# Performance work log

Hardware: AMD Instinct MI355X
Metric: run time of the kernel (lower is better)

The kernel has to match this reference:

```python
import jax, jax.numpy as jnp
import numpy as np
import math

B, T, C = 2, 1024, 1024
NEMBD = 1024
NATTN = 1024
NHEAD = 16
CTX = 1024
HS = NATTN // NHEAD          # head size = 64
ROT = HS // 2                # rotary dims = 32


def rotate_half(x):
    x1, x2 = x[..., : x.shape[-1] // 2], x[..., x.shape[-1] // 2 :]
    return jnp.concatenate((-x2, x1), axis=-1)


def setup_inputs() -> dict:
    key = jax.random.key(0)
    ks = jax.random.split(key, 16)
    s = 0.02
    inp = {
        "x": jax.random.normal(ks[0], (B, T, C), dtype=jnp.float32),
        # time-decay params (torch inits them to ones; add noise for a nontrivial test)
        "time_w": 1.0 + s * jax.random.normal(ks[1], (NHEAD, CTX), dtype=jnp.float32),
        "time_alpha": 1.0 + s * jax.random.normal(ks[2], (NHEAD, 1, CTX), dtype=jnp.float32),
        "time_beta": 1.0 + s * jax.random.normal(ks[3], (NHEAD, CTX, 1), dtype=jnp.float32),
        "time_gamma": 1.0 + s * jax.random.normal(ks[4], (CTX, 1), dtype=jnp.float32),
        # projections (stored as (in, out) for x @ W)
        "Wq": s * jax.random.normal(ks[5], (NEMBD, NATTN), dtype=jnp.float32),
        "bq": s * jax.random.normal(ks[6], (NATTN,), dtype=jnp.float32),
        "Wk": s * jax.random.normal(ks[7], (NEMBD, NATTN), dtype=jnp.float32),
        "bk": s * jax.random.normal(ks[8], (NATTN,), dtype=jnp.float32),
        "Wv": s * jax.random.normal(ks[9], (NEMBD, NATTN), dtype=jnp.float32),
        "bv": s * jax.random.normal(ks[10], (NATTN,), dtype=jnp.float32),
        # 1x1 conv over head channels: (out_head, in_head)
        "Wmix": s * jax.random.normal(ks[11], (NHEAD, NHEAD), dtype=jnp.float32),
        "Wo": s * jax.random.normal(ks[12], (NATTN, NEMBD), dtype=jnp.float32),
        "bo": s * jax.random.normal(ks[13], (NEMBD,), dtype=jnp.float32),
    }
    return inp


def reference(x, time_w, time_alpha, time_beta, time_gamma,
              Wq, bq, Wk, bk, Wv, bv, Wmix, Wo, bo):
    Bx, Tx, Cx = x.shape
    TT = CTX

    # --- relative time-decay weight matrix (H, T, T) ---
    w = jnp.pad(time_w, ((0, 0), (0, TT)))          # (H, 2TT)
    w = jnp.tile(w, (1, TT))                        # (H, 2TT*TT)
    w = w[:, :-TT].reshape(NHEAD, TT, 2 * TT - 1)
    w = w[:, :, TT - 1:]                            # (H, TT, TT)
    w = w[:, :Tx, :Tx] * time_alpha[:, :, :Tx] * time_beta[:, :Tx, :]

    # --- time shift of the first half of channels ---
    half = Cx // 2
    x_shift = jnp.pad(x[:, :, :half], ((0, 0), (1, 0), (0, 0)))[:, :Tx, :]
    xs = jnp.concatenate([x_shift, x[:, :, half:]], axis=-1)

    # --- q/k/v projections -> (B, H, T, hs) ---
    q = (xs @ Wq + bq).reshape(Bx, Tx, NHEAD, HS).transpose(0, 2, 1, 3)
    k = (xs @ Wk + bk).reshape(Bx, Tx, NHEAD, HS).transpose(0, 2, 1, 3)
    v = (xs @ Wv + bv).reshape(Bx, Tx, NHEAD, HS).transpose(0, 2, 1, 3)

    # --- rotary on the first ROT dims of each head (base = ctx_len) ---
    qr, q_pass = q[..., :ROT], q[..., ROT:]
    kr, k_pass = k[..., :ROT], k[..., ROT:]
    inv_freq = 1.0 / (jnp.float32(CTX) ** (jnp.arange(0, ROT, 2, dtype=jnp.float32) / ROT))
    t = jnp.arange(Tx, dtype=jnp.float32)
    freqs = t[:, None] * inv_freq[None, :]          # (T, ROT/2)
    emb = jnp.concatenate((freqs, freqs), axis=-1)  # (T, ROT)
    cos, sin = jnp.cos(emb), jnp.sin(emb)
    qr = qr * cos + rotate_half(qr) * sin
    kr = kr * cos + rotate_half(kr) * sin
    q = jnp.concatenate((qr, q_pass), axis=-1)
    k = jnp.concatenate((kr, k_pass), axis=-1)

    # --- attention with time decay and cross-head 1x1 mix ---
    att = jnp.einsum('bhtd,bhsd->bhts', q, k) * (1.0 / math.sqrt(HS))
    att = jax.nn.softmax(att, axis=-1)
    att = att * w[None]                              # (B,H,T,T) * (1,H,T,T)
    att = jnp.einsum('gh,bhts->bgts', Wmix, att)     # 1x1 conv over head channel
    y = jnp.einsum('bhts,bhsd->bhtd', att, v)
    y = y.transpose(0, 2, 1, 3).reshape(Bx, Tx, NATTN)
    return (y @ Wo + bo) * time_gamma[:Tx, :]
```

## Files before the change

kernel.cpp:

```cpp
#include <hip/hip_runtime.h>

typedef unsigned short u16;
typedef __attribute__((ext_vector_type(8))) short bf16x8;
typedef __attribute__((ext_vector_type(4))) float f32x4;

#define MFMA(a,b,c) __builtin_amdgcn_mfma_f32_16x16x32_bf16(a,b,c,0,0,0)

__device__ __forceinline__ float b2f(u16 u){
  union { unsigned int i; float f; } v; v.i = ((unsigned int)u)<<16; return v.f;
}
__device__ __forceinline__ u16 f2b(float f){
  union { float f; unsigned int i; } v; v.f = f;
  unsigned int r = (v.i + 0x7FFFu + ((v.i>>16)&1u))>>16;
  return (u16)r;
}

__global__ __launch_bounds__(256) void k_pre(
    const float* __restrict__ x,
    const float* __restrict__ Wq, const float* __restrict__ Wk,
    const float* __restrict__ Wv, const float* __restrict__ Wo,
    u16* __restrict__ xs, u16* __restrict__ WT, u16* __restrict__ WoT)
{
  int bid = blockIdx.x;
  int tid = threadIdx.x;
  if (bid < 1024){
    int idx = bid*256 + tid;
    size_t e = (size_t)idx*8;
    int c = (int)(e & 1023);
    int t = (int)((e>>10)&1023);
    float4 f0 = {0.f,0.f,0.f,0.f}, f1 = {0.f,0.f,0.f,0.f};
    const float* src = nullptr;
    if (c < 512){ if (t > 0) src = x + e - 1024; }
    else        { src = x + e; }
    if (src){ f0 = *(const float4*)src; f1 = *(const float4*)(src+4); }
    u16 o[8];
    o[0]=f2b(f0.x); o[1]=f2b(f0.y); o[2]=f2b(f0.z); o[3]=f2b(f0.w);
    o[4]=f2b(f1.x); o[5]=f2b(f1.y); o[6]=f2b(f1.z); o[7]=f2b(f1.w);
    *(uint4*)(xs + e) = *(const uint4*)o;
    return;
  }
  int z  = (bid-1024)>>8;
  int rc = (bid-1024)&255;
  const float* src = (z==0)?Wq:((z==1)?Wk:((z==2)?Wv:Wo));
  u16* dst = (z==3)? WoT : (WT + (size_t)z*1048576);
  int c0 = (rc&15)*64, r0 = (rc>>4)*64;
  __shared__ u16 tile[64][72];
  int r = tid>>2, cc = (tid&3)*16;
  const float* sp = src + (size_t)(r0+r)*1024 + c0+cc;
  float4 a0 = *(const float4*)(sp);
  float4 a1 = *(const float4*)(sp+4);
  float4 a2 = *(const float4*)(sp+8);
  float4 a3 = *(const float4*)(sp+12);
  tile[r][cc+0]=f2b(a0.x); tile[r][cc+1]=f2b(a0.y); tile[r][cc+2]=f2b(a0.z); tile[r][cc+3]=f2b(a0.w);
  tile[r][cc+4]=f2b(a1.x); tile[r][cc+5]=f2b(a1.y); tile[r][cc+6]=f2b(a1.z); tile[r][cc+7]=f2b(a1.w);
  tile[r][cc+8]=f2b(a2.x); tile[r][cc+9]=f2b(a2.y); tile[r][cc+10]=f2b(a2.z); tile[r][cc+11]=f2b(a2.w);
  tile[r][cc+12]=f2b(a3.x); tile[r][cc+13]=f2b(a3.y); tile[r][cc+14]=f2b(a3.z); tile[r][cc+15]=f2b(a3.w);
  __syncthreads();
  int c = tid>>2, rr = (tid&3)*16;
  uint4 o0,o1; u16* p0=(u16*)&o0; u16* p1=(u16*)&o1;
  #pragma unroll
  for (int i=0;i<8;i++){ p0[i]=tile[rr+i][c]; p1[i]=tile[rr+8+i][c]; }
  *(uint4*)(dst + (size_t)(c0+c)*1024 + r0+rr)   = o0;
  *(uint4*)(dst + (size_t)(c0+c)*1024 + r0+rr+8) = o1;
}

__global__ __launch_bounds__(256) void k_gemm_qkv(
    const u16* __restrict__ A, const u16* __restrict__ Bt,
    const float* __restrict__ bq, const float* __restrict__ bk, const float* __restrict__ bv,
    u16* __restrict__ qb, u16* __restrict__ kb, u16* __restrict__ vT)
{
  __shared__ u16 As[128*40];
  __shared__ u16 Bs[128*40];
  const int n0 = blockIdx.x*128, m0 = blockIdx.y*128;
  const int tid = threadIdx.x, lane = tid&63, wave = tid>>6;
  const int quad = lane>>4, l16 = lane&15;
  const int wm = (wave>>1)*64, wn = (wave&1)*64;
  f32x4 zero = {0.f,0.f,0.f,0.f};
  f32x4 acc[4][4];
  #pragma unroll
  for (int i=0;i<4;i++)
    #pragma unroll
    for (int j=0;j<4;j++) acc[i][j] = zero;
  const int row = tid>>1, kk = (tid&1)*16;
  const u16* pa = A  + (size_t)(m0+row)*1024 + kk;
  const u16* pb = Bt + (size_t)(n0+row)*1024 + kk;
  for (int k0=0;k0<1024;k0+=32){
    __syncthreads();
    uint4 a0 = *(const uint4*)(pa); uint4 a1 = *(const uint4*)(pa+8);
    uint4 b0 = *(const uint4*)(pb); uint4 b1 = *(const uint4*)(pb+8);
    pa += 32; pb += 32;
    *(uint4*)&As[row*40+kk] = a0; *(uint4*)&As[row*40+kk+8] = a1;
    *(uint4*)&Bs[row*40+kk] = b0; *(uint4*)&Bs[row*40+kk+8] = b1;
    __syncthreads();
    bf16x8 af[4], bfr[4];
    #pragma unroll
    for (int mt=0;mt<4;mt++) af[mt]  = *(const bf16x8*)&As[(wm+mt*16+l16)*40 + quad*8];
    #pragma unroll
    for (int nt=0;nt<4;nt++) bfr[nt] = *(const bf16x8*)&Bs[(wn+nt*16+l16)*40 + quad*8];
    #pragma unroll
    for (int mt=0;mt<4;mt++)
      #pragma unroll
      for (int nt=0;nt<4;nt++)
        acc[mt][nt] = MFMA(af[mt], bfr[nt], acc[mt][nt]);
  }
  const int colbase = n0 + wn;
  const int which = colbase>>10;
  const int nn0 = colbase & 1023;
  const int h = nn0>>6;
  const float* barr = (which==0)?bq:((which==1)?bk:bv);
  float bias[4];
  #pragma unroll
  for (int nt=0;nt<4;nt++) bias[nt] = barr[nn0 + nt*16 + l16];
  if (which == 2){
    #pragma unroll
    for (int mt=0;mt<4;mt++)
      #pragma unroll
      for (int r=0;r<4;r++){
        int m = m0 + wm + mt*16 + quad*4 + r;
        int bb = m>>10, t = m&1023;
        size_t base = (size_t)(bb*16+h)*65536 + t;
        #pragma unroll
        for (int nt=0;nt<4;nt++){
          int d = nt*16 + l16;
          vT[base + (size_t)d*1024] = f2b(acc[mt][nt][r] + bias[nt]);
        }
      }
  } else {
    const float scale = (which==0)?0.125f:1.0f;
    u16* dst = (which==0)? qb : kb;
    const float e = exp2f(-0.625f*(float)l16);
    #pragma unroll
    for (int mt=0;mt<4;mt++)
      #pragma unroll
      for (int r=0;r<4;r++){
        int m = m0 + wm + mt*16 + quad*4 + r;
        int bb = m>>10, t = m&1023;
        float f = (float)t * e;
        float cs = cosf(f), sn = sinf(f);
        float x0 = acc[mt][0][r] + bias[0];
        float x1 = acc[mt][1][r] + bias[1];
        float v0 = (x0*cs - x1*sn)*scale;
        float v1 = (x1*cs + x0*sn)*scale;
        float v2 = (acc[mt][2][r] + bias[2])*scale;
        float v3 = (acc[mt][3][r] + bias[3])*scale;
        size_t ob = (((size_t)(bb*16+h))*1024 + (size_t)t)*64 + l16;
        dst[ob]    = f2b(v0);
        dst[ob+16] = f2b(v1);
        dst[ob+32] = f2b(v2);
        dst[ob+48] = f2b(v3);
      }
  }
}

__global__ __launch_bounds__(256) void k_gemm_out(
    const u16* __restrict__ A, const u16* __restrict__ Bt,
    const float* __restrict__ bo, const float* __restrict__ gamma, float* __restrict__ out)
{
  __shared__ u16 As[128*40];
  __shared__ u16 Bs[128*40];
  const int n0 = blockIdx.x*128, m0 = blockIdx.y*128;
  const int tid = threadIdx.x, lane = tid&63, wave = tid>>6;
  const int quad = lane>>4, l16 = lane&15;
  const int wm = (wave>>1)*64, wn = (wave&1)*64;
  f32x4 zero = {0.f,0.f,0.f,0.f};
  f32x4 acc[4][4];
  #pragma unroll
  for (int i=0;i<4;i++)
    #pragma unroll
    for (int j=0;j<4;j++) acc[i][j] = zero;
  const int row = tid>>1, kk = (tid&1)*16;
  const u16* pa = A  + (size_t)(m0+row)*1024 + kk;
  const u16* pb = Bt + (size_t)(n0+row)*1024 + kk;
  for (int k0=0;k0<1024;k0+=32){
    __syncthreads();
    uint4 a0 = *(const uint4*)(pa); uint4 a1 = *(const uint4*)(pa+8);
    uint4 b0 = *(const uint4*)(pb); uint4 b1 = *(const uint4*)(pb+8);
    pa += 32; pb += 32;
    *(uint4*)&As[row*40+kk] = a0; *(uint4*)&As[row*40+kk+8] = a1;
    *(uint4*)&Bs[row*40+kk] = b0; *(uint4*)&Bs[row*40+kk+8] = b1;
    __syncthreads();
    bf16x8 af[4], bfr[4];
    #pragma unroll
    for (int mt=0;mt<4;mt++) af[mt]  = *(const bf16x8*)&As[(wm+mt*16+l16)*40 + quad*8];
    #pragma unroll
    for (int nt=0;nt<4;nt++) bfr[nt] = *(const bf16x8*)&Bs[(wn+nt*16+l16)*40 + quad*8];
    #pragma unroll
    for (int mt=0;mt<4;mt++)
      #pragma unroll
      for (int nt=0;nt<4;nt++)
        acc[mt][nt] = MFMA(af[mt], bfr[nt], acc[mt][nt]);
  }
  #pragma unroll
  for (int mt=0;mt<4;mt++)
    #pragma unroll
    for (int nt=0;nt<4;nt++){
      int colg = n0 + wn + nt*16 + l16;
      float bias = bo[colg];
      #pragma unroll
      for (int r=0;r<4;r++){
        int m = m0 + wm + mt*16 + quad*4 + r;
        int t = m&1023;
        float val = (acc[mt][nt][r] + bias)*gamma[t];
        out[(size_t)m*1024 + colg] = val;
      }
    }
}

__global__ __launch_bounds__(1024) void k_sm(
    const u16* __restrict__ q, const u16* __restrict__ k,
    const float* __restrict__ tw, const float* __restrict__ alpha, const float* __restrict__ beta,
    u16* __restrict__ P)
{
  const int tb = blockIdx.x, h = blockIdx.y, b = blockIdx.z;
  const int t0b = tb*64;
  const int tid = threadIdx.x;
  const int wave = tid>>6, lane = tid&63, quad = lane>>4, l16 = lane&15;
  const int wt = wave>>2, ws = wave&3;

  __shared__ u16 qs[64*76];
  __shared__ u16 ks[256*76];
  __shared__ float tws[1024];
  __shared__ float als[1024];
  __shared__ float pm[4][64];
  __shared__ float pl[4][64];
  __shared__ float fm[64];
  __shared__ float fr[64];

  const size_t bh = (size_t)(b*16+h)*65536;
  const u16* qp = q + bh;
  const u16* kp = k + bh;

  if (tid < 512){
    int row = tid>>3, g = tid&7;
    *(uint4*)&qs[row*76 + g*8] = *(const uint4*)(qp + (size_t)(t0b+row)*64 + g*8);
  }
  tws[tid] = tw[h*1024 + tid];
  als[tid] = alpha[h*1024 + tid];
  __syncthreads();

  bf16x8 qf0 = *(const bf16x8*)&qs[(wt*16+l16)*76 + quad*8];
  bf16x8 qf1 = *(const bf16x8*)&qs[(wt*16+l16)*76 + quad*8 + 32];

  f32x4 acc[16];
  #pragma unroll
  for (int i=0;i<16;i++){ acc[i][0]=0.f; acc[i][1]=0.f; acc[i][2]=0.f; acc[i][3]=0.f; }

  #pragma unroll
  for (int c=0;c<4;c++){
    if (c) __syncthreads();
    {
      int row = tid>>3, g = tid&7;
      *(uint4*)&ks[row*76 + g*8]       = *(const uint4*)(kp + (size_t)(c*256+row)*64 + g*8);
      *(uint4*)&ks[(row+128)*76 + g*8] = *(const uint4*)(kp + (size_t)(c*256+row+128)*64 + g*8);
    }
    __syncthreads();
    #pragma unroll
    for (int j=0;j<4;j++){
      int lt = j*4 + ws;
      bf16x8 kf0 = *(const bf16x8*)&ks[(lt*16+l16)*76 + quad*8];
      bf16x8 kf1 = *(const bf16x8*)&ks[(lt*16+l16)*76 + quad*8 + 32];
      acc[c*4+j] = MFMA(qf0, kf0, acc[c*4+j]);
      acc[c*4+j] = MFMA(qf1, kf1, acc[c*4+j]);
    }
  }

  float mrow[4], lrow[4];
  #pragma unroll
  for (int r=0;r<4;r++){
    float m = acc[0][r];
    #pragma unroll
    for (int a=1;a<16;a++) m = fmaxf(m, acc[a][r]);
    #pragma unroll
    for (int off=1; off<16; off<<=1) m = fmaxf(m, __shfl_xor(m, off));
    float l = 0.f;
    #pragma unroll
    for (int a=0;a<16;a++) l += __expf(acc[a][r]-m);
    #pragma unroll
    for (int off=1; off<16; off<<=1) l += __shfl_xor(l, off);
    mrow[r]=m; lrow[r]=l;
  }
  if (l16==0){
    #pragma unroll
    for (int r=0;r<4;r++){
      pm[ws][wt*16+quad*4+r] = mrow[r];
      pl[ws][wt*16+quad*4+r] = lrow[r];
    }
  }
  __syncthreads();
  if (tid < 64){
    float m0s = pm[0][tid], m1s = pm[1][tid], m2s = pm[2][tid], m3s = pm[3][tid];
    float m = fmaxf(fmaxf(m0s,m1s), fmaxf(m2s,m3s));
    float l = pl[0][tid]*__expf(m0s-m) + pl[1][tid]*__expf(m1s-m)
            + pl[2][tid]*__expf(m2s-m) + pl[3][tid]*__expf(m3s-m);
    fm[tid] = m;
    fr[tid] = beta[h*1024 + t0b + tid] / l;
  }
  __syncthreads();

  u16* Pp = P + ((size_t)(b*16+h)<<20);
  float m_f[4], r_f[4]; int trow[4];
  #pragma unroll
  for (int r=0;r<4;r++){
    int rg = wt*16+quad*4+r;
    m_f[r] = fm[rg]; r_f[r] = fr[rg]; trow[r] = t0b + rg;
  }
  const int slim = tb*4 + wt;
  #pragma unroll
  for (int c=0;c<4;c++)
    #pragma unroll
    for (int j=0;j<4;j++){
      int st = c*16 + j*4 + ws;
      if (st > slim) continue;
      int s = st*16 + l16;
      float av = als[s];
      #pragma unroll
      for (int r=0;r<4;r++){
        int t = trow[r];
        float p = 0.f;
        if (s <= t)
          p = __expf(acc[c*4+j][r]-m_f[r])*r_f[r]*tws[1023+s-t]*av;
        Pp[((size_t)t<<10) + s] = f2b(p);
      }
    }
}

__global__ __launch_bounds__(256) void k_mix(const u16* __restrict__ P, const float* __restrict__ Wm,
                                             u16* __restrict__ Ab)
{
  int tid = threadIdx.x;
  int b = blockIdx.z;
  int t = blockIdx.x*4 + (tid>>6);
  int sb = blockIdx.y*256 + (tid&63)*4;
  int tmaxw = t|31, tmaxr = t|15;
  if ((int)(blockIdx.y*256) > tmaxw) return;
  __shared__ float Wl[16][16];
  Wl[tid>>4 & 15][tid&15] = Wm[tid & 255];
  __syncthreads();
  const u16* Pb = P  + ((size_t)(b*16)<<20);
  u16* Abb      = Ab + ((size_t)(b*16)<<20);
  float a[16][4];
  #pragma unroll
  for (int g=0;g<16;g++){ a[g][0]=0.f; a[g][1]=0.f; a[g][2]=0.f; a[g][3]=0.f; }
  #pragma unroll
  for (int h=0;h<16;h++){
    float p0=0.f,p1=0.f,p2=0.f,p3=0.f;
    if (sb <= tmaxr){
      ushort4 u = *(const ushort4*)(Pb + (((size_t)h)<<20) + (((size_t)t)<<10) + sb);
      p0=b2f(u.x); p1=b2f(u.y); p2=b2f(u.z); p3=b2f(u.w);
    }
    #pragma unroll
    for (int g=0;g<16;g++){
      float w = Wl[g][h];
      a[g][0]+=w*p0; a[g][1]+=w*p1; a[g][2]+=w*p2; a[g][3]+=w*p3;
    }
  }
  if (sb <= tmaxw){
    #pragma unroll
    for (int g=0;g<16;g++){
      ushort4 o; o.x=f2b(a[g][0]); o.y=f2b(a[g][1]); o.z=f2b(a[g][2]); o.w=f2b(a[g][3]);
      *(ushort4*)(Abb + (((size_t)g)<<20) + (((size_t)t)<<10) + sb) = o;
    }
  }
}

__global__ __launch_bounds__(1024) void k_pv(const u16* __restrict__ Ab, const u16* __restrict__ vT,
                                             u16* __restrict__ y)
{
  const int tb = blockIdx.x;
  const int bg = blockIdx.y;
  const int b = bg>>4, g = bg&15;
  const int t0b = tb*64;
  const int tid = threadIdx.x;
  const int wave = tid>>6, lane = tid&63, quad = lane>>4, l16 = lane&15;
  const int wt = wave>>2, wd = wave&3;
  __shared__ u16 As[64*264];
  __shared__ u16 Vs[64*264];
  const u16* ap = Ab + ((size_t)bg<<20);
  const u16* vp = vT + (size_t)bg*65536;
  f32x4 acc = {0.f,0.f,0.f,0.f};
  const int nc = tb/4 + 1;
  const int row = tid>>4, col = (tid&15)*16;
  for (int c=0;c<nc;c++){
    if (c) __syncthreads();
    int s0 = c*256;
    *(uint4*)&As[row*264+col]   = *(const uint4*)(ap + (((size_t)(t0b+row))<<10) + s0+col);
    *(uint4*)&As[row*264+col+8] = *(const uint4*)(ap + (((size_t)(t0b+row))<<10) + s0+col+8);
    *(uint4*)&Vs[row*264+col]   = *(const uint4*)(vp + (size_t)row*1024 + s0+col);
    *(uint4*)&Vs[row*264+col+8] = *(const uint4*)(vp + (size_t)row*1024 + s0+col+8);
    __syncthreads();
    #pragma unroll
    for (int ks=0;ks<8;ks++){
      bf16x8 af  = *(const bf16x8*)&As[(wt*16+l16)*264 + ks*32 + quad*8];
      bf16x8 bfv = *(const bf16x8*)&Vs[(wd*16+l16)*264 + ks*32 + quad*8];
      acc = MFMA(af, bfv, acc);
    }
  }
  #pragma unroll
  for (int r=0;r<4;r++){
    int t = t0b + wt*16 + quad*4 + r;
    y[(size_t)(b*1024+t)*1024 + g*64 + wd*16 + l16] = f2b(acc[r]);
  }
}

__global__ void k_fail(float* out){ if (threadIdx.x==0) out[0] = 1e30f; }

extern "C" void kernel_launch(void* const* d_in, const int* in_sizes, int n_in,
                              void* d_out, int out_size, void* d_ws, size_t ws_size,
                              hipStream_t stream)
{
  const float* x     = (const float*)d_in[0];
  const float* tw    = (const float*)d_in[1];
  const float* alpha = (const float*)d_in[2];
  const float* beta  = (const float*)d_in[3];
  const float* gamma = (const float*)d_in[4];
  const float* Wq    = (const float*)d_in[5];
  const float* bq    = (const float*)d_in[6];
  const float* Wk    = (const float*)d_in[7];
  const float* bk    = (const float*)d_in[8];
  const float* Wv    = (const float*)d_in[9];
  const float* bv    = (const float*)d_in[10];
  const float* Wmix  = (const float*)d_in[11];
  const float* Wo    = (const float*)d_in[12];
  const float* bo    = (const float*)d_in[13];
  float* out = (float*)d_out;

  char* ws = (char*)d_ws;
  size_t off = 0;
  auto take = [&](size_t bytes)->char*{
    char* p = ws + off; off += (bytes + 255) & ~(size_t)255; return p;
  };
  u16*   xs  = (u16*)take((size_t)2097152*2);
  u16*   WT  = (u16*)take((size_t)3145728*2);
  u16*   WoT = (u16*)take((size_t)1048576*2);
  u16*   qb  = (u16*)take((size_t)2097152*2);
  u16*   kb  = (u16*)take((size_t)2097152*2);
  u16*   vTb = (u16*)take((size_t)2097152*2);
  u16*   yb  = (u16*)take((size_t)2097152*2);
  u16*   P   = (u16*)take((size_t)33554432*2);
  u16*   A   = (u16*)take((size_t)33554432*2);
  if (off > ws_size){
    hipLaunchKernelGGL(k_fail, dim3(1), dim3(64), 0, stream, out);
    return;
  }

  hipLaunchKernelGGL(k_pre, dim3(2048), dim3(256), 0, stream,
                     x, Wq, Wk, Wv, Wo, xs, WT, WoT);
  hipLaunchKernelGGL(k_gemm_qkv, dim3(24,16), dim3(256), 0, stream,
                     xs, WT, bq, bk, bv, qb, kb, vTb);
  hipLaunchKernelGGL(k_sm, dim3(16,16,2), dim3(1024), 0, stream,
                     qb, kb, tw, alpha, beta, P);
  hipLaunchKernelGGL(k_mix, dim3(256,4,2), dim3(256), 0, stream, P, Wmix, A);
  hipLaunchKernelGGL(k_pv, dim3(16,32), dim3(1024), 0, stream, A, vTb, yb);
  hipLaunchKernelGGL(k_gemm_out, dim3(8,16), dim3(256), 0, stream, yb, WoT, bo, gamma, out);
}
```

Measured before the change: 243.1 us.

## Store attention probabilities head-interleaved per row and restage head mix through LDS

Changes the layout of the P and A attention buffers from [b][h][t][s] to [b][t][h][s], so all 16 heads for one query row sit together in a contiguous 32KB slab. The head-mix kernel now runs one block per (t,b), loads that slab into shared memory with 16-byte loads, keeps each output head's mix weights in registers, and writes coalesced 16-element vectors. The aim is better coalescing and locality in the mix step. The cost is more blocks, a larger row stride for k_sm writes and k_pv reads, and writes of zero chunks beyond the causal bound.

```diff
diff --git a/kernel.cpp b/kernel.cpp
--- a/kernel.cpp
+++ b/kernel.cpp
@@ -297,7 +297,7 @@
   }
   __syncthreads();
 
-  u16* Pp = P + ((size_t)(b*16+h)<<20);
+  u16* Pp = P + (((size_t)b)<<24) + (((size_t)h)<<10);
   float m_f[4], r_f[4]; int trow[4];
   #pragma unroll
   for (int r=0;r<4;r++){
@@ -319,7 +319,7 @@
         float p = 0.f;
         if (s <= t)
           p = __expf(acc[c*4+j][r]-m_f[r])*r_f[r]*tws[1023+s-t]*av;
-        Pp[((size_t)t<<10) + s] = f2b(p);
+        Pp[((size_t)t<<14) + s] = f2b(p);
       }
     }
 }
@@ -327,38 +327,56 @@
 __global__ __launch_bounds__(256) void k_mix(const u16* __restrict__ P, const float* __restrict__ Wm,
                                              u16* __restrict__ Ab)
 {
-  int tid = threadIdx.x;
-  int b = blockIdx.z;
-  int t = blockIdx.x*4 + (tid>>6);
-  int sb = blockIdx.y*256 + (tid&63)*4;
-  int tmaxw = t|31, tmaxr = t|15;
-  if ((int)(blockIdx.y*256) > tmaxw) return;
-  __shared__ float Wl[16][16];
-  Wl[tid>>4 & 15][tid&15] = Wm[tid & 255];
-  __syncthreads();
-  const u16* Pb = P  + ((size_t)(b*16)<<20);
-  u16* Abb      = Ab + ((size_t)(b*16)<<20);
-  float a[16][4];
-  #pragma unroll
-  for (int g=0;g<16;g++){ a[g][0]=0.f; a[g][1]=0.f; a[g][2]=0.f; a[g][3]=0.f; }
-  #pragma unroll
-  for (int h=0;h<16;h++){
-    float p0=0.f,p1=0.f,p2=0.f,p3=0.f;
-    if (sb <= tmaxr){
-      ushort4 u = *(const ushort4*)(Pb + (((size_t)h)<<20) + (((size_t)t)<<10) + sb);
-      p0=b2f(u.x); p1=b2f(u.y); p2=b2f(u.z); p3=b2f(u.w);
-    }
-    #pragma unroll
-    for (int g=0;g<16;g++){
-      float w = Wl[g][h];
-      a[g][0]+=w*p0; a[g][1]+=w*p1; a[g][2]+=w*p2; a[g][3]+=w*p3;
-    }
-  }
-  if (sb <= tmaxw){
-    #pragma unroll
-    for (int g=0;g<16;g++){
-      ushort4 o; o.x=f2b(a[g][0]); o.y=f2b(a[g][1]); o.z=f2b(a[g][2]); o.w=f2b(a[g][3]);
-      *(ushort4*)(Abb + (((size_t)g)<<20) + (((size_t)t)<<10) + sb) = o;
+  const int t = blockIdx.x, b = blockIdx.y;
+  const int tid = threadIdx.x;
+  const int g = tid>>4, sg = tid&15;
+  __shared__ u16 Ps[16*264];
+  float w[16];
+  #pragma unroll
+  for (int h=0;h<16;h++) w[h] = Wm[g*16+h];
+  const int tmaxr = t|15;
+  const int ncw = (t>>8) + 1;
+  const size_t slab = (((size_t)b)<<24) + (((size_t)t)<<14);
+  const u16* pp = P + slab;
+  u16* ap = Ab + slab;
+  for (int c=0;c<ncw;c++){
+    int s0 = c*256;
+    if (s0 <= tmaxr){
+      if (c) __syncthreads();
+      int colg = sg*16;
+      uint4 z = {0u,0u,0u,0u};
+      uint4 v0 = z, v1 = z;
+      if (s0+colg <= tmaxr){
+        v0 = *(const uint4*)(pp + ((size_t)g<<10) + s0+colg);
+        v1 = *(const uint4*)(pp + ((size_t)g<<10) + s0+colg+8);
+      }
+      *(uint4*)&Ps[g*264+colg]   = v0;
+      *(uint4*)&Ps[g*264+colg+8] = v1;
+      __syncthreads();
+      float acc[16];
+      #pragma unroll
+      for (int i=0;i<16;i++) acc[i]=0.f;
+      #pragma unroll
+      for (int h=0;h<16;h++){
+        float wh = w[h];
+        #pragma unroll
+        for (int j=0;j<4;j++){
+          ushort4 u = *(const ushort4*)&Ps[h*264 + sg*16 + j*4];
+          acc[j*4+0] += wh*b2f(u.x);
+          acc[j*4+1] += wh*b2f(u.y);
+          acc[j*4+2] += wh*b2f(u.z);
+          acc[j*4+3] += wh*b2f(u.w);
+        }
+      }
+      u16 o[16];
+      #pragma unroll
+      for (int i=0;i<16;i++) o[i] = f2b(acc[i]);
+      *(uint4*)(ap + ((size_t)g<<10) + s0 + sg*16)     = *(uint4*)&o[0];
+      *(uint4*)(ap + ((size_t)g<<10) + s0 + sg*16 + 8) = *(uint4*)&o[8];
+    } else {
+      uint4 z = {0u,0u,0u,0u};
+      *(uint4*)(ap + ((size_t)g<<10) + s0 + sg*16)     = z;
+      *(uint4*)(ap + ((size_t)g<<10) + s0 + sg*16 + 8) = z;
     }
   }
 }
@@ -375,7 +393,7 @@
   const int wt = wave>>2, wd = wave&3;
   __shared__ u16 As[64*264];
   __shared__ u16 Vs[64*264];
-  const u16* ap = Ab + ((size_t)bg<<20);
+  const u16* ap = Ab + (((size_t)b)<<24) + ((size_t)g<<10);
   const u16* vp = vT + (size_t)bg*65536;
   f32x4 acc = {0.f,0.f,0.f,0.f};
   const int nc = tb/4 + 1;
@@ -383,8 +401,8 @@
   for (int c=0;c<nc;c++){
     if (c) __syncthreads();
     int s0 = c*256;
-    *(uint4*)&As[row*264+col]   = *(const uint4*)(ap + (((size_t)(t0b+row))<<10) + s0+col);
-    *(uint4*)&As[row*264+col+8] = *(const uint4*)(ap + (((size_t)(t0b+row))<<10) + s0+col+8);
+    *(uint4*)&As[row*264+col]   = *(const uint4*)(ap + ((size_t)(t0b+row)<<14) + s0+col);
+    *(uint4*)&As[row*264+col+8] = *(const uint4*)(ap + ((size_t)(t0b+row)<<14) + s0+col+8);
     *(uint4*)&Vs[row*264+col]   = *(const uint4*)(vp + (size_t)row*1024 + s0+col);
     *(uint4*)&Vs[row*264+col+8] = *(const uint4*)(vp + (size_t)row*1024 + s0+col+8);
     __syncthreads();
@@ -449,7 +467,7 @@
                      xs, WT, bq, bk, bv, qb, kb, vTb);
   hipLaunchKernelGGL(k_sm, dim3(16,16,2), dim3(1024), 0, stream,
                      qb, kb, tw, alpha, beta, P);
-  hipLaunchKernelGGL(k_mix, dim3(256,4,2), dim3(256), 0, stream, P, Wmix, A);
+  hipLaunchKernelGGL(k_mix, dim3(1024,2), dim3(256), 0, stream, P, Wmix, A);
   hipLaunchKernelGGL(k_pv, dim3(16,32), dim3(1024), 0, stream, A, vTb, yb);
   hipLaunchKernelGGL(k_gemm_out, dim3(8,16), dim3(256), 0, stream, yb, WoT, bo, gamma, out);
 }
```

Result: faster. 228.3 us (-6.1%).
